# Kernel optimization log

Measured on AMD Instinct MI355X. Metric: run time of the kernel, lower is better.

Reference implementation:

```python
import jax, jax.numpy as jnp
import numpy as np

N = 50000      # nodes
E = 800000     # edges
IN = 256       # in_feats
H = 4          # num_heads
F = 64         # out_feats
K = 3          # hops
SLOPE = 0.2    # leaky_relu negative slope


def setup_inputs() -> dict:
    key = jax.random.key(0)
    ks = jax.random.split(key, 9)
    feat = jax.random.normal(ks[0], (N, IN), jnp.float32)
    src = jax.random.randint(ks[1], (E,), 0, N, dtype=jnp.int32)
    dst = jax.random.randint(ks[2], (E,), 0, N, dtype=jnp.int32)
    W = jax.random.normal(ks[3], (IN, H * F), jnp.float32) * (1.0 / np.sqrt(IN))
    attn_l = jax.random.normal(ks[4], (1, H, F), jnp.float32) * 0.1
    attn_r = jax.random.normal(ks[5], (1, H, F), jnp.float32) * 0.1
    hop_attn_l = jax.random.normal(ks[6], (1, H, F), jnp.float32) * 0.1
    hop_attn_r = jax.random.normal(ks[7], (1, H, F), jnp.float32) * 0.1
    sigma = jax.random.uniform(ks[8], (1,), jnp.float32)
    return dict(feat=feat, src=src, dst=dst, W=W, attn_l=attn_l, attn_r=attn_r,
                hop_attn_l=hop_attn_l, hop_attn_r=hop_attn_r, sigma=sigma)


def _edge_softmax(e, idx, n):
    # softmax over edges grouped by node index `idx` (src- or dst-grouped)
    m = jax.ops.segment_max(e, idx, num_segments=n)          # (N,H,1)
    ex = jnp.exp(e - m[idx])                                 # (E,H,1), stable
    s = jax.ops.segment_sum(ex, idx, num_segments=n)         # (N,H,1)
    return ex / s[idx]


def _forward(feat, W, attn_l, attn_r, hop_attn_l, hop_attn_r, sigma, src, dst):
    h = (feat @ W).reshape(N, H, F)                          # fc, view
    el = (h * attn_l).sum(-1, keepdims=True)                 # (N,H,1)
    er = (h * attn_r).sum(-1, keepdims=True)
    e = jax.nn.leaky_relu(el[src] + er[dst], SLOPE)          # (E,H,1)
    # dual edge-softmax with learned mixing exponent (norm='both')
    a_src = jnp.clip(_edge_softmax(e, src, N), 1e-10)
    a_dst = jnp.clip(_edge_softmax(e, dst, N), 1e-10)
    s = jax.nn.sigmoid(sigma[0])
    a = (a_dst ** s) * (a_src ** (1.0 - s))                  # (E,H,1)
    # GCN-style degree norms
    ones = jnp.ones((E,), jnp.float32)
    out_deg = jnp.clip(jax.ops.segment_sum(ones, src, num_segments=N), 1.0)
    in_deg = jnp.clip(jax.ops.segment_sum(ones, dst, num_segments=N), 1.0)
    norm_out = (out_deg ** -0.5)[:, None, None]
    norm_in = (in_deg ** 0.5)[:, None, None]
    hstack = [h]
    x = h
    for _ in range(K):
        xs = x * norm_out
        msg = xs[src] * a                                    # (E,H,F) u_mul_e
        x = jax.ops.segment_sum(msg, dst, num_segments=N) * norm_in
        hstack.append(x)
    # hop attention combination
    a_l = (h * hop_attn_l).sum(-1, keepdims=True)            # (N,H,1)
    astack = jnp.stack(
        [a_l + (fd * hop_attn_r).sum(-1, keepdims=True) for fd in hstack],
        axis=-1)                                             # (N,H,1,K+1)
    ha = jax.nn.softmax(jax.nn.leaky_relu(astack, SLOPE), axis=-1)
    rst = sum(hstack[i] * ha[..., i] for i in range(K + 1))  # (N,H,F)
    return rst


def reference(feat, src, dst, W, attn_l, attn_r, hop_attn_l, hop_attn_r, sigma):
    return _forward(feat, W, attn_l, attn_r, hop_attn_l, hop_attn_r, sigma, src, dst)
```

## Files before the change

### kernel.cpp

```cpp
#include <hip/hip_runtime.h>
#include <hip/hip_bf16.h>

#define N_NODES 50000
#define N_EDGES 800000
#define HF      256
#define SLOPE   0.2f
#define BIN_W   1024
#define NBINS   49

static inline size_t align256(size_t x) { return (x + 255) & ~(size_t)255; }

__device__ __forceinline__ float lrelu(float x) { return x > 0.f ? x : SLOPE * x; }

__device__ __forceinline__ float bf2f(unsigned short b) {
  return __uint_as_float(((unsigned)b) << 16);
}
__device__ __forceinline__ unsigned short f2bf(float f) {
  unsigned u = __float_as_uint(f);
  unsigned r = (u + 0x7FFFu + ((u >> 16) & 1u)) >> 16;
  return (unsigned short)r;
}

using f32x4 = __attribute__((ext_vector_type(4))) float;
using s16x8 = __attribute__((ext_vector_type(8))) short;

__global__ __launch_bounds__(256) void w_swizzle(
    const float* __restrict__ W, unsigned short* __restrict__ W_swz) {
  int t = blockIdx.x * 256 + threadIdx.x;
  int k = t >> 8, col = t & 255;
  int kin = k & 31, chunk = k >> 5;
  int tile = col >> 4;
  int lane = ((kin >> 3) << 4) | (col & 15);
  int j = kin & 7;
  W_swz[(((chunk * 16 + tile) * 64 + lane) << 3) + j] = f2bf(W[t]);
}

__global__ __launch_bounds__(256) void mfma_gemm(
    const float* __restrict__ feat, const unsigned short* __restrict__ W_swz,
    unsigned short* __restrict__ h_bf,
    const float* __restrict__ attn_l, const float* __restrict__ attn_r,
    const float* __restrict__ hop_attn_l,
    float* __restrict__ el, float* __restrict__ er, float* __restrict__ al) {
  __shared__ unsigned short sW[32768];
  int tid = threadIdx.x;
  int w = tid >> 6, lane = tid & 63;
  int c15 = lane & 15, g = lane >> 4;
  int wave_row = blockIdx.x * 64 + w * 16;
  int row_a = wave_row + c15;
  bool va = row_a < N_NODES;

  float4 av[16];
  const float* ap = feat + (size_t)row_a * 256 + g * 8;
#pragma unroll
  for (int c = 0; c < 8; ++c) {
    if (va) {
      av[2 * c]     = *(const float4*)(ap + c * 32);
      av[2 * c + 1] = *(const float4*)(ap + c * 32 + 4);
    } else {
      av[2 * c] = make_float4(0.f, 0.f, 0.f, 0.f);
      av[2 * c + 1] = av[2 * c];
    }
  }

  f32x4 acc[16];
#pragma unroll
  for (int t = 0; t < 16; ++t) acc[t] = (f32x4){0.f, 0.f, 0.f, 0.f};

  const s16x8* sWf = (const s16x8*)sW;
#pragma unroll
  for (int hf = 0; hf < 2; ++hf) {
    if (hf) __syncthreads();
    {
      const uint4* gw = (const uint4*)(W_swz + hf * 32768);
      uint4* sw4 = (uint4*)sW;
      for (int i = tid; i < 4096; i += 256) sw4[i] = gw[i];
    }
    __syncthreads();
#pragma unroll
    for (int cc = 0; cc < 4; ++cc) {
      int c = hf * 4 + cc;
      s16x8 a;
      const float* p0 = (const float*)&av[2 * c];
#pragma unroll
      for (int j = 0; j < 8; ++j) a[j] = (short)f2bf(p0[j]);
#pragma unroll
      for (int t = 0; t < 16; ++t) {
        s16x8 b = sWf[(cc * 16 + t) * 64 + lane];
        acc[t] = __builtin_amdgcn_mfma_f32_16x16x32_bf16(a, b, acc[t], 0, 0, 0);
      }
    }
  }

  float pl[16], pr[16], pa[16];
#pragma unroll
  for (int i = 0; i < 16; ++i) { pl[i] = 0.f; pr[i] = 0.f; pa[i] = 0.f; }
#pragma unroll
  for (int t = 0; t < 16; ++t) {
    int colv = t * 16 + c15;
    float la = attn_l[colv], ra = attn_r[colv], ha = hop_attn_l[colv];
    int h = t >> 2;
#pragma unroll
    for (int r = 0; r < 4; ++r) {
      pl[r * 4 + h] = fmaf(acc[t][r], la, pl[r * 4 + h]);
      pr[r * 4 + h] = fmaf(acc[t][r], ra, pr[r * 4 + h]);
      pa[r * 4 + h] = fmaf(acc[t][r], ha, pa[r * 4 + h]);
    }
  }
#pragma unroll
  for (int i = 0; i < 16; ++i) {
#pragma unroll
    for (int off = 8; off; off >>= 1) {
      pl[i] += __shfl_xor(pl[i], off);
      pr[i] += __shfl_xor(pr[i], off);
      pa[i] += __shfl_xor(pa[i], off);
    }
  }
  int rowg = wave_row + g * 4;
  if (c15 == 0) {
#pragma unroll
    for (int r = 0; r < 4; ++r) {
      if (rowg + r < N_NODES) {
        *(float4*)&el[(rowg + r) * 4] = make_float4(pl[r*4+0], pl[r*4+1], pl[r*4+2], pl[r*4+3]);
        *(float4*)&er[(rowg + r) * 4] = make_float4(pr[r*4+0], pr[r*4+1], pr[r*4+2], pr[r*4+3]);
        *(float4*)&al[(rowg + r) * 4] = make_float4(pa[r*4+0], pa[r*4+1], pa[r*4+2], pa[r*4+3]);
      }
    }
  }
#pragma unroll
  for (int r = 0; r < 4; ++r) {
    int row = rowg + r;
    if (row < N_NODES) {
#pragma unroll
      for (int t = 0; t < 16; ++t) {
        h_bf[(size_t)row * HF + t * 16 + c15] = f2bf(acc[t][r]);
      }
    }
  }
}

__global__ __launch_bounds__(256) void bin_hist(
    const int* __restrict__ src, const int* __restrict__ dst,
    int* __restrict__ binA, int* __restrict__ binB) {
  __shared__ int cA[NBINS], cB[NBINS];
  int t = threadIdx.x;
  if (t < NBINS) { cA[t] = 0; cB[t] = 0; }
  __syncthreads();
  int e = blockIdx.x * 256 + t;
  int s = src[e], d = dst[e];
  atomicAdd(&cA[d >> 10], 1);
  atomicAdd(&cB[s >> 10], 1);
  __syncthreads();
  if (t < NBINS) {
    if (cA[t]) atomicAdd(&binA[t], cA[t]);
    if (cB[t]) atomicAdd(&binB[t], cB[t]);
  }
}

__global__ void bin_scan(const int* __restrict__ binA, const int* __restrict__ binB,
                         int* __restrict__ baseA, int* __restrict__ baseB,
                         int* __restrict__ allocA, int* __restrict__ allocB,
                         int* __restrict__ row_ptr, int* __restrict__ col_ptr) {
  int t = threadIdx.x;
  int vA = (t < NBINS) ? binA[t] : 0;
  int vB = (t < NBINS) ? binB[t] : 0;
  int xA = vA, xB = vB;
#pragma unroll
  for (int off = 1; off < 64; off <<= 1) {
    int yA = __shfl_up(xA, off);
    int yB = __shfl_up(xB, off);
    if (t >= off) { xA += yA; xB += yB; }
  }
  if (t < NBINS) {
    baseA[t] = xA - vA; allocA[t] = xA - vA;
    baseB[t] = xB - vB; allocB[t] = xB - vB;
  }
  if (t == NBINS - 1) {
    baseA[NBINS] = xA; baseB[NBINS] = xB;
    row_ptr[N_NODES] = N_EDGES; col_ptr[N_NODES] = N_EDGES;
  }
}

__global__ __launch_bounds__(256) void bin_scatter(
    const int* __restrict__ src, const int* __restrict__ dst,
    int* __restrict__ allocA, int* __restrict__ allocB,
    int2* __restrict__ recA, int2* __restrict__ recB) {
  __shared__ int cA[NBINS], cB[NBINS], bA[NBINS], bB[NBINS];
  int t = threadIdx.x;
  if (t < NBINS) { cA[t] = 0; cB[t] = 0; }
  __syncthreads();
  int e = blockIdx.x * 256 + t;
  int s = src[e], d = dst[e];
  int ba = d >> 10, bb = s >> 10;
  int ra = atomicAdd(&cA[ba], 1);
  int rb = atomicAdd(&cB[bb], 1);
  __syncthreads();
  if (t < NBINS) {
    bA[t] = cA[t] ? atomicAdd(&allocA[t], cA[t]) : 0;
    bB[t] = cB[t] ? atomicAdd(&allocB[t], cB[t]) : 0;
  }
  __syncthreads();
  recA[bA[ba] + ra] = make_int2(s, d);
  recB[bB[bb] + rb] = make_int2(d, s);
}

__global__ __launch_bounds__(256) void bin_sort(
    const int2* __restrict__ recA, const int* __restrict__ baseA,
    int* __restrict__ row_ptr, int* __restrict__ outA,
    const int2* __restrict__ recB, const int* __restrict__ baseB,
    int* __restrict__ col_ptr, int* __restrict__ outB) {
  const int2* rec; const int* base; int* ptr; int* out;
  if (blockIdx.y == 0) { rec = recA; base = baseA; ptr = row_ptr; out = outA; }
  else                 { rec = recB; base = baseB; ptr = col_ptr; out = outB; }
  __shared__ int hist[BIN_W];
  __shared__ int wsum[4];
  int b = blockIdx.x, t = threadIdx.x;
  int n0 = b << 10;
  int nn = min(BIN_W, N_NODES - n0);
  int beg = base[b], end = base[b + 1];
  for (int i = t; i < BIN_W; i += 256) hist[i] = 0;
  __syncthreads();
  for (int p = beg + t; p < end; p += 256)
    atomicAdd(&hist[rec[p].y - n0], 1);
  __syncthreads();
  int i0 = t * 4;
  int h0 = hist[i0], h1 = hist[i0 + 1], h2 = hist[i0 + 2], h3 = hist[i0 + 3];
  int sum4 = h0 + h1 + h2 + h3;
  int x = sum4;
  int lane = t & 63, wid = t >> 6;
#pragma unroll
  for (int off = 1; off < 64; off <<= 1) {
    int y = __shfl_up(x, off);
    if (lane >= off) x += y;
  }
  if (lane == 63) wsum[wid] = x;
  __syncthreads();
  int wpre = 0;
#pragma unroll
  for (int wj = 0; wj < 4; ++wj) wpre += (wj < wid) ? wsum[wj] : 0;
  int excl = wpre + x - sum4;
  int e0 = excl, e1 = excl + h0, e2 = excl + h0 + h1, e3 = excl + h0 + h1 + h2;
  hist[i0] = e0; hist[i0 + 1] = e1; hist[i0 + 2] = e2; hist[i0 + 3] = e3;
  if (i0 + 0 < nn) ptr[n0 + i0 + 0] = beg + e0;
  if (i0 + 1 < nn) ptr[n0 + i0 + 1] = beg + e1;
  if (i0 + 2 < nn) ptr[n0 + i0 + 2] = beg + e2;
  if (i0 + 3 < nn) ptr[n0 + i0 + 3] = beg + e3;
  __syncthreads();
  for (int p = beg + t; p < end; p += 256) {
    int2 r = rec[p];
    int pos = atomicAdd(&hist[r.y - n0], 1);
    out[beg + pos] = r.x;
  }
}

__global__ void norm_in_kernel(const int* __restrict__ row_ptr, float* __restrict__ norm_in) {
  int n = blockIdx.x * blockDim.x + threadIdx.x;
  if (n >= N_NODES) return;
  int deg = row_ptr[n + 1] - row_ptr[n];
  norm_in[n] = sqrtf((float)max(deg, 1));
}

__global__ __launch_bounds__(256) void src_coef(
    const int* __restrict__ col_ptr, const int* __restrict__ row,
    const float4* __restrict__ el4, const float4* __restrict__ er4,
    const float* __restrict__ sigma, float4* __restrict__ cs4) {
  int n = (int)(((size_t)blockIdx.x * blockDim.x + threadIdx.x) >> 6);
  int lane = threadIdx.x & 63;
  if (n >= N_NODES) return;
  int beg = col_ptr[n], end = col_ptr[n + 1];
  float4 o = el4[n];
  float s0 = 0.f, s1 = 0.f, s2 = 0.f, s3 = 0.f;
  for (int p = beg + lane; p < end; p += 64) {
    int u = row[p];
    float4 e = er4[u];
    s0 += __expf(lrelu(e.x + o.x));
    s1 += __expf(lrelu(e.y + o.y));
    s2 += __expf(lrelu(e.z + o.z));
    s3 += __expf(lrelu(e.w + o.w));
  }
#pragma unroll
  for (int off = 32; off; off >>= 1) {
    s0 += __shfl_xor(s0, off); s1 += __shfl_xor(s1, off);
    s2 += __shfl_xor(s2, off); s3 += __shfl_xor(s3, off);
  }
  if (lane == 0) {
    float sg = 1.f / (1.f + __expf(-sigma[0]));
    float c = 0.5f * __logf((float)max(end - beg, 1));
    float k = 1.f - sg;
    cs4[n] = make_float4(k * __logf(s0) + c, k * __logf(s1) + c,
                         k * __logf(s2) + c, k * __logf(s3) + c);
  }
}

__global__ __launch_bounds__(256) void csr_weights(
    const int* __restrict__ row_ptr, const int* __restrict__ col,
    const float4* __restrict__ el4, const float4* __restrict__ er4,
    const float4* __restrict__ cs4, const float* __restrict__ sigma,
    float4* __restrict__ w4) {
  int d = (int)(((size_t)blockIdx.x * blockDim.x + threadIdx.x) >> 6);
  int lane = threadIdx.x & 63;
  if (d >= N_NODES) return;
  int beg = row_ptr[d], end = row_ptr[d + 1];
  if (beg == end) return;
  float4 o = er4[d];
  float s0 = 0.f, s1 = 0.f, s2 = 0.f, s3 = 0.f;
  for (int p = beg + lane; p < end; p += 64) {
    int s_ = col[p];
    float4 e = el4[s_];
    s0 += __expf(lrelu(e.x + o.x));
    s1 += __expf(lrelu(e.y + o.y));
    s2 += __expf(lrelu(e.z + o.z));
    s3 += __expf(lrelu(e.w + o.w));
  }
#pragma unroll
  for (int off = 32; off; off >>= 1) {
    s0 += __shfl_xor(s0, off); s1 += __shfl_xor(s1, off);
    s2 += __shfl_xor(s2, off); s3 += __shfl_xor(s3, off);
  }
  float sg = 1.f / (1.f + __expf(-sigma[0]));
  float c0 = sg * __logf(s0), c1 = sg * __logf(s1);
  float c2 = sg * __logf(s2), c3 = sg * __logf(s3);
  for (int p = beg + lane; p < end; p += 64) {
    int s_ = col[p];
    float4 e = el4[s_];
    float4 cc = cs4[s_];
    float4 wv;
    wv.x = __expf(lrelu(e.x + o.x) - c0 - cc.x);
    wv.y = __expf(lrelu(e.y + o.y) - c1 - cc.y);
    wv.z = __expf(lrelu(e.z + o.z) - c2 - cc.z);
    wv.w = __expf(lrelu(e.w + o.w) - c3 - cc.w);
    w4[p] = wv;
  }
}

__global__ __launch_bounds__(256) void hop_kernel(
    const unsigned short* __restrict__ xin, unsigned short* __restrict__ xout,
    const int* __restrict__ row_ptr, const int* __restrict__ col,
    const float* __restrict__ w, const float* __restrict__ norm_in) {
  int d = (int)(((size_t)blockIdx.x * blockDim.x + threadIdx.x) >> 6);
  int lane = threadIdx.x & 63;
  if (d >= N_NODES) return;
  int hh = lane >> 4;
  int beg = row_ptr[d], end = row_ptr[d + 1];
  float a0 = 0.f, a1 = 0.f, a2 = 0.f, a3 = 0.f;
  const unsigned short* xl = xin + lane * 4;
  int p = beg;
  for (; p + 3 < end; p += 4) {
    int s0 = col[p], s1 = col[p + 1], s2 = col[p + 2], s3 = col[p + 3];
    float w0 = w[(size_t)p * 4 + hh];
    float w1 = w[(size_t)p * 4 + 4 + hh];
    float w2 = w[(size_t)p * 4 + 8 + hh];
    float w3 = w[(size_t)p * 4 + 12 + hh];
    ushort4 u0 = *(const ushort4*)(xl + (size_t)s0 * HF);
    ushort4 u1 = *(const ushort4*)(xl + (size_t)s1 * HF);
    ushort4 u2 = *(const ushort4*)(xl + (size_t)s2 * HF);
    ushort4 u3 = *(const ushort4*)(xl + (size_t)s3 * HF);
    a0 = fmaf(w0, bf2f(u0.x), a0); a1 = fmaf(w0, bf2f(u0.y), a1);
    a2 = fmaf(w0, bf2f(u0.z), a2); a3 = fmaf(w0, bf2f(u0.w), a3);
    a0 = fmaf(w1, bf2f(u1.x), a0); a1 = fmaf(w1, bf2f(u1.y), a1);
    a2 = fmaf(w1, bf2f(u1.z), a2); a3 = fmaf(w1, bf2f(u1.w), a3);
    a0 = fmaf(w2, bf2f(u2.x), a0); a1 = fmaf(w2, bf2f(u2.y), a1);
    a2 = fmaf(w2, bf2f(u2.z), a2); a3 = fmaf(w2, bf2f(u2.w), a3);
    a0 = fmaf(w3, bf2f(u3.x), a0); a1 = fmaf(w3, bf2f(u3.y), a1);
    a2 = fmaf(w3, bf2f(u3.z), a2); a3 = fmaf(w3, bf2f(u3.w), a3);
  }
  for (; p < end; ++p) {
    int s = col[p];
    float wt = w[(size_t)p * 4 + hh];
    ushort4 u = *(const ushort4*)(xl + (size_t)s * HF);
    a0 = fmaf(wt, bf2f(u.x), a0); a1 = fmaf(wt, bf2f(u.y), a1);
    a2 = fmaf(wt, bf2f(u.z), a2); a3 = fmaf(wt, bf2f(u.w), a3);
  }
  float ni = norm_in[d];
  ushort4 o;
  o.x = f2bf(a0 * ni); o.y = f2bf(a1 * ni);
  o.z = f2bf(a2 * ni); o.w = f2bf(a3 * ni);
  *(ushort4*)&xout[(size_t)d * HF + lane * 4] = o;
}

__global__ __launch_bounds__(256) void final_combine(
    const unsigned short* __restrict__ h0, const unsigned short* __restrict__ x1,
    const unsigned short* __restrict__ x2, const unsigned short* __restrict__ x3,
    const float* __restrict__ al, const float* __restrict__ hop_attn_r,
    float* __restrict__ out) {
  int n = blockIdx.x, t = threadIdx.x;
  size_t idx = (size_t)n * HF + t;
  float v0 = bf2f(h0[idx]), v1 = bf2f(x1[idx]), v2 = bf2f(x2[idx]), v3 = bf2f(x3[idx]);
  float wr = hop_attn_r[t];
  float b0 = v0 * wr, b1 = v1 * wr, b2 = v2 * wr, b3 = v3 * wr;
#pragma unroll
  for (int off = 32; off; off >>= 1) {
    b0 += __shfl_xor(b0, off);
    b1 += __shfl_xor(b1, off);
    b2 += __shfl_xor(b2, off);
    b3 += __shfl_xor(b3, off);
  }
  float a0 = al[n * 4 + (t >> 6)];
  b0 = lrelu(b0 + a0); b1 = lrelu(b1 + a0); b2 = lrelu(b2 + a0); b3 = lrelu(b3 + a0);
  float m = fmaxf(fmaxf(b0, b1), fmaxf(b2, b3));
  float e0 = expf(b0 - m), e1 = expf(b1 - m), e2 = expf(b2 - m), e3 = expf(b3 - m);
  float inv = 1.f / (e0 + e1 + e2 + e3);
  out[idx] = (v0 * e0 + v1 * e1 + v2 * e2 + v3 * e3) * inv;
}

extern "C" void kernel_launch(void* const* d_in, const int* in_sizes, int n_in,
                              void* d_out, int out_size, void* d_ws, size_t ws_size,
                              hipStream_t stream) {
  const float* feat       = (const float*)d_in[0];
  const int*   src        = (const int*)d_in[1];
  const int*   dst        = (const int*)d_in[2];
  const float* W          = (const float*)d_in[3];
  const float* attn_l     = (const float*)d_in[4];
  const float* attn_r     = (const float*)d_in[5];
  const float* hop_attn_l = (const float*)d_in[6];
  const float* hop_attn_r = (const float*)d_in[7];
  const float* sigma      = (const float*)d_in[8];
  float* out = (float*)d_out;

  char* ws = (char*)d_ws;
  size_t off = 0;
  auto alloc = [&](size_t bytes) -> void* {
    void* p = ws + off;
    off = align256(off + bytes);
    return p;
  };
  unsigned short* h_bf  = (unsigned short*)alloc((size_t)N_NODES * HF * 2);
  unsigned short* x1    = (unsigned short*)alloc((size_t)N_NODES * HF * 2);
  unsigned short* x2    = (unsigned short*)alloc((size_t)N_NODES * HF * 2);
  unsigned short* x3    = (unsigned short*)alloc((size_t)N_NODES * HF * 2);
  float* w_csr  = (float*)alloc((size_t)N_EDGES * 4 * 4);
  int*   col    = (int*)alloc((size_t)N_EDGES * 4);
  int*   row    = (int*)alloc((size_t)N_EDGES * 4);
  int*   row_ptr= (int*)alloc((size_t)(N_NODES + 1) * 4);
  int*   col_ptr= (int*)alloc((size_t)(N_NODES + 1) * 4);
  float* el     = (float*)alloc((size_t)N_NODES * 4 * 4);
  float* er     = (float*)alloc((size_t)N_NODES * 4 * 4);
  float* al     = (float*)alloc((size_t)N_NODES * 4 * 4);
  float* cs     = (float*)alloc((size_t)N_NODES * 4 * 4);
  float* norm_in= (float*)alloc((size_t)N_NODES * 4);
  unsigned short* W_swz = (unsigned short*)alloc((size_t)65536 * 2);
  int* baseA    = (int*)alloc((size_t)(NBINS + 1) * 4);
  int* baseB    = (int*)alloc((size_t)(NBINS + 1) * 4);
  int* allocA   = (int*)alloc((size_t)NBINS * 4);
  int* allocB   = (int*)alloc((size_t)NBINS * 4);
  size_t zoff = off;
  int* binA     = (int*)alloc((size_t)NBINS * 4);
  int* binB     = (int*)alloc((size_t)NBINS * 4);
  size_t zbytes = off - zoff;
  int2* recA = (int2*)x1;
  int2* recB = (int2*)x2;

  hipMemsetAsync(ws + zoff, 0, zbytes, stream);

  w_swizzle<<<256, 256, 0, stream>>>(W, W_swz);
  mfma_gemm<<<(N_NODES + 63) / 64, 256, 0, stream>>>(
      feat, W_swz, h_bf, attn_l, attn_r, hop_attn_l, el, er, al);
  const int EB = N_EDGES / 256;
  bin_hist<<<EB, 256, 0, stream>>>(src, dst, binA, binB);
  bin_scan<<<1, 64, 0, stream>>>(binA, binB, baseA, baseB, allocA, allocB, row_ptr, col_ptr);
  bin_scatter<<<EB, 256, 0, stream>>>(src, dst, allocA, allocB, recA, recB);
  bin_sort<<<dim3(NBINS, 2), 256, 0, stream>>>(recA, baseA, row_ptr, col,
                                               recB, baseB, col_ptr, row);
  norm_in_kernel<<<(N_NODES + 255) / 256, 256, 0, stream>>>(row_ptr, norm_in);
  const int HB = (N_NODES * 64 + 255) / 256;
  src_coef<<<HB, 256, 0, stream>>>(col_ptr, row, (const float4*)el, (const float4*)er,
                                   sigma, (float4*)cs);
  csr_weights<<<HB, 256, 0, stream>>>(row_ptr, col, (const float4*)el, (const float4*)er,
                                      (const float4*)cs, sigma, (float4*)w_csr);
  hop_kernel<<<HB, 256, 0, stream>>>(h_bf, x1, row_ptr, col, w_csr, norm_in);
  hop_kernel<<<HB, 256, 0, stream>>>(x1, x2, row_ptr, col, w_csr, norm_in);
  hop_kernel<<<HB, 256, 0, stream>>>(x2, x3, row_ptr, col, w_csr, norm_in);
  final_combine<<<N_NODES, 256, 0, stream>>>(h_bf, x1, x2, x3, al, hop_attn_r, out);
}
```

Before: 604.1 us.

## Split bin counters into sub-slots and unroll hop gather by eight

Each bin's global histogram and allocation counter becomes 32 sub-counters, selected by block index. This spreads the atomic contention across the 3125 edge blocks, and a new two-block scan kernel replaces the single-wave scan to build the offsets. The hop kernel also gains an 8-way unrolled gather loop so more independent loads are in flight per wavefront. The cost is extra scan work and higher register pressure in hop_kernel.

```diff
diff --git a/kernel.cpp b/kernel.cpp
--- a/kernel.cpp
+++ b/kernel.cpp
@@ -7,6 +7,7 @@
 #define SLOPE   0.2f
 #define BIN_W   1024
 #define NBINS   49
+#define G_SUB   32
 
 static inline size_t align256(size_t x) { return (x + 255) & ~(size_t)255; }
 
@@ -140,7 +141,7 @@
 
 __global__ __launch_bounds__(256) void bin_hist(
     const int* __restrict__ src, const int* __restrict__ dst,
-    int* __restrict__ binA, int* __restrict__ binB) {
+    int* __restrict__ cntA, int* __restrict__ cntB) {
   __shared__ int cA[NBINS], cB[NBINS];
   int t = threadIdx.x;
   if (t < NBINS) { cA[t] = 0; cB[t] = 0; }
@@ -150,39 +151,69 @@
   atomicAdd(&cA[d >> 10], 1);
   atomicAdd(&cB[s >> 10], 1);
   __syncthreads();
+  int g = blockIdx.x & (G_SUB - 1);
   if (t < NBINS) {
-    if (cA[t]) atomicAdd(&binA[t], cA[t]);
-    if (cB[t]) atomicAdd(&binB[t], cB[t]);
-  }
-}
-
-__global__ void bin_scan(const int* __restrict__ binA, const int* __restrict__ binB,
-                         int* __restrict__ baseA, int* __restrict__ baseB,
-                         int* __restrict__ allocA, int* __restrict__ allocB,
-                         int* __restrict__ row_ptr, int* __restrict__ col_ptr) {
-  int t = threadIdx.x;
-  int vA = (t < NBINS) ? binA[t] : 0;
-  int vB = (t < NBINS) ? binB[t] : 0;
-  int xA = vA, xB = vB;
-#pragma unroll
-  for (int off = 1; off < 64; off <<= 1) {
-    int yA = __shfl_up(xA, off);
-    int yB = __shfl_up(xB, off);
-    if (t >= off) { xA += yA; xB += yB; }
-  }
-  if (t < NBINS) {
-    baseA[t] = xA - vA; allocA[t] = xA - vA;
-    baseB[t] = xB - vB; allocB[t] = xB - vB;
-  }
-  if (t == NBINS - 1) {
-    baseA[NBINS] = xA; baseB[NBINS] = xB;
-    row_ptr[N_NODES] = N_EDGES; col_ptr[N_NODES] = N_EDGES;
+    if (cA[t]) atomicAdd(&cntA[t * G_SUB + g], cA[t]);
+    if (cB[t]) atomicAdd(&cntB[t * G_SUB + g], cB[t]);
+  }
+}
+
+__global__ __launch_bounds__(1024) void scan2(
+    const int* __restrict__ cntA, int* __restrict__ curA, int* __restrict__ baseA,
+    const int* __restrict__ cntB, int* __restrict__ curB, int* __restrict__ baseB,
+    int* __restrict__ row_ptr, int* __restrict__ col_ptr) {
+  const int* cnt = (blockIdx.x == 0) ? cntA : cntB;
+  int* cur  = (blockIdx.x == 0) ? curA : curB;
+  int* base = (blockIdx.x == 0) ? baseA : baseB;
+  __shared__ int wsum[16];
+  __shared__ int carry_s;
+  if (threadIdx.x == 0) carry_s = 0;
+  __syncthreads();
+  const int NTOT = NBINS * G_SUB;
+  for (int b0 = 0; b0 < NTOT; b0 += 1024) {
+    int i = b0 + threadIdx.x;
+    int v = (i < NTOT) ? cnt[i] : 0;
+    int lane = threadIdx.x & 63, wid = threadIdx.x >> 6;
+    int x = v;
+#pragma unroll
+    for (int off = 1; off < 64; off <<= 1) {
+      int y = __shfl_up(x, off, 64);
+      if (lane >= off) x += y;
+    }
+    if (lane == 63) wsum[wid] = x;
+    __syncthreads();
+    if (threadIdx.x < 16) {
+      int s = wsum[threadIdx.x];
+#pragma unroll
+      for (int off = 1; off < 16; off <<= 1) {
+        int y = __shfl_up(s, off, 16);
+        if ((int)(threadIdx.x & 15) >= off) s += y;
+      }
+      wsum[threadIdx.x] = s;
+    }
+    __syncthreads();
+    int carry = carry_s;
+    int pre = (wid > 0) ? wsum[wid - 1] : 0;
+    int incl = x + pre + carry;
+    int excl = incl - v;
+    if (i < NTOT) {
+      cur[i] = excl;
+      if ((i & (G_SUB - 1)) == 0) base[i / G_SUB] = excl;
+    }
+    __syncthreads();
+    if (threadIdx.x == 1023) carry_s = incl;
+    __syncthreads();
+  }
+  if (threadIdx.x == 0) {
+    base[NBINS] = N_EDGES;
+    if (blockIdx.x == 0) row_ptr[N_NODES] = N_EDGES;
+    else                 col_ptr[N_NODES] = N_EDGES;
   }
 }
 
 __global__ __launch_bounds__(256) void bin_scatter(
     const int* __restrict__ src, const int* __restrict__ dst,
-    int* __restrict__ allocA, int* __restrict__ allocB,
+    int* __restrict__ curA, int* __restrict__ curB,
     int2* __restrict__ recA, int2* __restrict__ recB) {
   __shared__ int cA[NBINS], cB[NBINS], bA[NBINS], bB[NBINS];
   int t = threadIdx.x;
@@ -194,9 +225,10 @@
   int ra = atomicAdd(&cA[ba], 1);
   int rb = atomicAdd(&cB[bb], 1);
   __syncthreads();
+  int g = blockIdx.x & (G_SUB - 1);
   if (t < NBINS) {
-    bA[t] = cA[t] ? atomicAdd(&allocA[t], cA[t]) : 0;
-    bB[t] = cB[t] ? atomicAdd(&allocB[t], cB[t]) : 0;
+    bA[t] = cA[t] ? atomicAdd(&curA[t * G_SUB + g], cA[t]) : 0;
+    bB[t] = cB[t] ? atomicAdd(&curB[t * G_SUB + g], cB[t]) : 0;
   }
   __syncthreads();
   recA[bA[ba] + ra] = make_int2(s, d);
@@ -344,6 +376,24 @@
   float a0 = 0.f, a1 = 0.f, a2 = 0.f, a3 = 0.f;
   const unsigned short* xl = xin + lane * 4;
   int p = beg;
+  for (; p + 7 < end; p += 8) {
+    int sv[8];
+    float wv[8];
+    ushort4 uv[8];
+#pragma unroll
+    for (int k = 0; k < 8; ++k) sv[k] = col[p + k];
+#pragma unroll
+    for (int k = 0; k < 8; ++k) wv[k] = w[(size_t)(p + k) * 4 + hh];
+#pragma unroll
+    for (int k = 0; k < 8; ++k) uv[k] = *(const ushort4*)(xl + (size_t)sv[k] * HF);
+#pragma unroll
+    for (int k = 0; k < 8; ++k) {
+      a0 = fmaf(wv[k], bf2f(uv[k].x), a0);
+      a1 = fmaf(wv[k], bf2f(uv[k].y), a1);
+      a2 = fmaf(wv[k], bf2f(uv[k].z), a2);
+      a3 = fmaf(wv[k], bf2f(uv[k].w), a3);
+    }
+  }
   for (; p + 3 < end; p += 4) {
     int s0 = col[p], s1 = col[p + 1], s2 = col[p + 2], s3 = col[p + 3];
     float w0 = w[(size_t)p * 4 + hh];
@@ -440,11 +490,11 @@
   unsigned short* W_swz = (unsigned short*)alloc((size_t)65536 * 2);
   int* baseA    = (int*)alloc((size_t)(NBINS + 1) * 4);
   int* baseB    = (int*)alloc((size_t)(NBINS + 1) * 4);
-  int* allocA   = (int*)alloc((size_t)NBINS * 4);
-  int* allocB   = (int*)alloc((size_t)NBINS * 4);
+  int* curA     = (int*)alloc((size_t)NBINS * G_SUB * 4);
+  int* curB     = (int*)alloc((size_t)NBINS * G_SUB * 4);
   size_t zoff = off;
-  int* binA     = (int*)alloc((size_t)NBINS * 4);
-  int* binB     = (int*)alloc((size_t)NBINS * 4);
+  int* cntA     = (int*)alloc((size_t)NBINS * G_SUB * 4);
+  int* cntB     = (int*)alloc((size_t)NBINS * G_SUB * 4);
   size_t zbytes = off - zoff;
   int2* recA = (int2*)x1;
   int2* recB = (int2*)x2;
@@ -455,9 +505,9 @@
   mfma_gemm<<<(N_NODES + 63) / 64, 256, 0, stream>>>(
       feat, W_swz, h_bf, attn_l, attn_r, hop_attn_l, el, er, al);
   const int EB = N_EDGES / 256;
-  bin_hist<<<EB, 256, 0, stream>>>(src, dst, binA, binB);
-  bin_scan<<<1, 64, 0, stream>>>(binA, binB, baseA, baseB, allocA, allocB, row_ptr, col_ptr);
-  bin_scatter<<<EB, 256, 0, stream>>>(src, dst, allocA, allocB, recA, recB);
+  bin_hist<<<EB, 256, 0, stream>>>(src, dst, cntA, cntB);
+  scan2<<<2, 1024, 0, stream>>>(cntA, curA, baseA, cntB, curB, baseB, row_ptr, col_ptr);
+  bin_scatter<<<EB, 256, 0, stream>>>(src, dst, curA, curB, recA, recB);
   bin_sort<<<dim3(NBINS, 2), 256, 0, stream>>>(recA, baseA, row_ptr, col,
                                                recB, baseB, col_ptr, row);
   norm_in_kernel<<<(N_NODES + 255) / 256, 256, 0, stream>>>(row_ptr, norm_in);
```

New measurement: 544.3 us. 1.11x faster.
